# Kernel optimization log

Hardware: AMD Instinct MI355X
Metric: run time of the kernel (lower is better)

## Reference

```python
import jax, jax.numpy as jnp
import numpy as np

N, D, H = 4096, 2048, 16
DK = D // H  # 128


def setup_inputs() -> dict:
    key = jax.random.key(0)
    k0, k1, k2, k3 = jax.random.split(key, 4)
    return {
        "tokens_embedding": jax.random.normal(k0, (N, D), dtype=jnp.float32),
        "w_q": jax.random.normal(k1, (H, D, DK), dtype=jnp.float32),
        "w_k": jax.random.normal(k2, (H, D, DK), dtype=jnp.float32),
        "w_v": jax.random.normal(k3, (H, D, DK), dtype=jnp.float32),
    }


def reference(tokens_embedding, w_q, w_k, w_v):
    # Per-head projections (batched over heads): [H, N, DK]
    q = jnp.einsum('nd,hdk->hnk', tokens_embedding, w_q)
    k = jnp.einsum('nd,hdk->hnk', tokens_embedding, w_k)
    v = jnp.einsum('nd,hdk->hnk', tokens_embedding, w_v)
    # Scaled dot-product attention, softmax over keys (orig dim=1 of [N,N])
    scale = 1.0 / jnp.sqrt(jnp.float32(DK))
    scores = jnp.einsum('hnk,hmk->hnm', q, k) * scale  # [H, N, N]
    attn = jax.nn.softmax(scores, axis=-1)
    out = jnp.einsum('hnm,hmk->hnk', attn, v)  # [H, N, DK]
    # Concat heads along feature dim (head order preserved): [N, H*DK]
    return jnp.transpose(out, (1, 0, 2)).reshape(N, H * DK)
```

## Files before the change

kernel.cpp:

```cpp
#include <hip/hip_runtime.h>
#include <hip/hip_bf16.h>

#define N_TOK 4096
#define D_MODEL 2048
#define NHEAD 16
#define DKH 128

typedef __attribute__((ext_vector_type(8))) short short8v;
typedef __attribute__((ext_vector_type(4))) float f32x4;
typedef __attribute__((ext_vector_type(8))) unsigned short ush8;

static __device__ __forceinline__ unsigned short f2bf(float f) {
  unsigned int x = __float_as_uint(f);
  return (unsigned short)((x + 0x7fffu + ((x >> 16) & 1u)) >> 16);
}
static __device__ __forceinline__ float bf2f(unsigned short u) {
  return __uint_as_float(((unsigned int)u) << 16);
}

static __device__ __forceinline__ void gld16(const void* g, void* l) {
  __builtin_amdgcn_global_load_lds(
      (const __attribute__((address_space(1))) unsigned int*)g,
      (__attribute__((address_space(3))) unsigned int*)l, 16, 0, 0);
}

__global__ __launch_bounds__(256)
void split_e_kernel(const float* __restrict__ E,
                    unsigned short* __restrict__ Eh,
                    unsigned short* __restrict__ El) {
  const size_t i = ((size_t)blockIdx.x * 256 + threadIdx.x) * 8;
  const int n = (int)(i >> 11), d0 = (int)(i & 2047);
  float4 v0 = *reinterpret_cast<const float4*>(E + i);
  float4 v1 = *reinterpret_cast<const float4*>(E + i + 4);
  float f[8] = {v0.x, v0.y, v0.z, v0.w, v1.x, v1.y, v1.z, v1.w};
  ush8 hi, lo;
#pragma unroll
  for (int j = 0; j < 8; ++j) {
    unsigned short hu = f2bf(f[j]);
    hi[j] = hu;
    lo[j] = f2bf(f[j] - bf2f(hu));
  }
  const size_t off = (size_t)n * D_MODEL + (d0 ^ ((n & 7) << 3));
  *reinterpret_cast<ush8*>(Eh + off) = hi;
  *reinterpret_cast<ush8*>(El + off) = lo;
}

__global__ __launch_bounds__(256)
void split_w_kernel(const float* __restrict__ Wq, const float* __restrict__ Wk,
                    const float* __restrict__ Wv,
                    unsigned short* __restrict__ WTh,
                    unsigned short* __restrict__ WTl) {
  __shared__ float tile[64][65];
  const int t = threadIdx.x;
  const int d0 = blockIdx.x * 64;
  const int k0 = blockIdx.y * 64;
  const int mh = blockIdx.z;
  const int mat = mh >> 4, h = mh & 15;
  const float* W = (mat == 0) ? Wq : (mat == 1) ? Wk : Wv;
  const float* Wp = W + (size_t)h * D_MODEL * DKH;
  const float fac = (mat == 0) ? (1.44269504089f / sqrtf(128.0f)) : 1.0f;

  const int rr = t >> 4, c4 = (t & 15) * 4;
#pragma unroll
  for (int p = 0; p < 4; ++p) {
    float4 v = *reinterpret_cast<const float4*>(Wp + (size_t)(d0 + rr + 16 * p) * DKH + k0 + c4);
    tile[rr + 16 * p][c4 + 0] = v.x * fac;
    tile[rr + 16 * p][c4 + 1] = v.y * fac;
    tile[rr + 16 * p][c4 + 2] = v.z * fac;
    tile[rr + 16 * p][c4 + 3] = v.w * fac;
  }
  __syncthreads();
  const int dd0 = (t & 7) * 8, kl = t >> 3;
#pragma unroll
  for (int p = 0; p < 2; ++p) {
    const int kg = k0 + kl + 32 * p;
    ush8 hi, lo;
#pragma unroll
    for (int j = 0; j < 8; ++j) {
      float f = tile[dd0 + j][kl + 32 * p];
      unsigned short hu = f2bf(f);
      hi[j] = hu;
      lo[j] = f2bf(f - bf2f(hu));
    }
    const size_t base = ((size_t)(mat * NHEAD + h) * DKH + kg) * D_MODEL +
                        d0 + (dd0 ^ ((kg & 7) << 3));
    *reinterpret_cast<ush8*>(WTh + base) = hi;
    if (mat < 2) *reinterpret_cast<ush8*>(WTl + base) = lo;
  }
}

template <int MODE>
__global__ __launch_bounds__(256, 2)
void proj_gemm_kernel(const unsigned short* __restrict__ Eh,
                      const unsigned short* __restrict__ El,
                      const unsigned short* __restrict__ WTh,
                      const unsigned short* __restrict__ WTl,
                      unsigned short* __restrict__ Qhi, unsigned short* __restrict__ Qlo,
                      unsigned short* __restrict__ Khi, unsigned short* __restrict__ Klo,
                      unsigned short* __restrict__ Vt, int h0) {
  __shared__ alignas(16) unsigned short Ah[128 * 64];
  __shared__ alignas(16) unsigned short Bh[128 * 64];
  __shared__ alignas(16) unsigned short Al[MODE == 0 ? 128 * 64 : 16];
  __shared__ alignas(16) unsigned short Bl[MODE == 0 ? 128 * 64 : 16];

  const int t = threadIdx.x;
  const int nb = blockIdx.x, hl = blockIdx.y, h = h0 + hl;
  const int mat = (MODE == 0) ? blockIdx.z : 2;
  const int wv = t >> 6, lane = t & 63, fr = lane & 15, fq = lane >> 4;
  const int m0 = (wv >> 1) * 64, n0 = (wv & 1) * 64;

  const char *pAh, *pBh, *pAl = nullptr, *pBl = nullptr;
  if (MODE == 0) {
    pAh = (const char*)(Eh + (size_t)nb * 128 * D_MODEL);
    pAl = (const char*)(El + (size_t)nb * 128 * D_MODEL);
    pBh = (const char*)(WTh + ((size_t)mat * NHEAD + h) * DKH * D_MODEL);
    pBl = (const char*)(WTl + ((size_t)mat * NHEAD + h) * DKH * D_MODEL);
  } else {
    pAh = (const char*)(WTh + ((size_t)2 * NHEAD + h) * DKH * D_MODEL);
    pBh = (const char*)(Eh + (size_t)nb * 128 * D_MODEL);
  }

  f32x4 acc[4][4];
#pragma unroll
  for (int a = 0; a < 4; ++a)
#pragma unroll
    for (int b = 0; b < 4; ++b) acc[a][b] = f32x4{0.f, 0.f, 0.f, 0.f};

  for (int d0 = 0; d0 < D_MODEL; d0 += 64) {
    __syncthreads();
    {
      const size_t gb = (size_t)d0 * 2 + (size_t)(t >> 3) * 4096 + (t & 7) * 16;
#pragma unroll
      for (int j = 0; j < 4; ++j) {
        gld16(pAh + gb + (size_t)j * 32 * 4096, (char*)Ah + j * 4096 + t * 16);
        gld16(pBh + gb + (size_t)j * 32 * 4096, (char*)Bh + j * 4096 + t * 16);
      }
      if (MODE == 0) {
#pragma unroll
        for (int j = 0; j < 4; ++j) {
          gld16(pAl + gb + (size_t)j * 32 * 4096, (char*)Al + j * 4096 + t * 16);
          gld16(pBl + gb + (size_t)j * 32 * 4096, (char*)Bl + j * 4096 + t * 16);
        }
      }
    }
    __syncthreads();
    __builtin_amdgcn_s_setprio(1);
#pragma unroll
    for (int ks = 0; ks < 2; ++ks) {
      short8v ah[4], al[4];
#pragma unroll
      for (int mi = 0; mi < 4; ++mi) {
        const int r = m0 + 16 * mi + fr;
        const int off = (ks * 32 + fq * 8) ^ ((r & 7) << 3);
        ah[mi] = *reinterpret_cast<const short8v*>(&Ah[r * 64 + off]);
        if (MODE == 0) al[mi] = *reinterpret_cast<const short8v*>(&Al[r * 64 + off]);
      }
#pragma unroll
      for (int ni = 0; ni < 4; ++ni) {
        const int rn = n0 + 16 * ni + fr;
        const int offn = (ks * 32 + fq * 8) ^ ((rn & 7) << 3);
        short8v bh = *reinterpret_cast<const short8v*>(&Bh[rn * 64 + offn]);
        if (MODE == 0) {
          short8v bl = *reinterpret_cast<const short8v*>(&Bl[rn * 64 + offn]);
#pragma unroll
          for (int mi = 0; mi < 4; ++mi) {
            acc[mi][ni] = __builtin_amdgcn_mfma_f32_16x16x32_bf16(ah[mi], bh, acc[mi][ni], 0, 0, 0);
            acc[mi][ni] = __builtin_amdgcn_mfma_f32_16x16x32_bf16(ah[mi], bl, acc[mi][ni], 0, 0, 0);
            acc[mi][ni] = __builtin_amdgcn_mfma_f32_16x16x32_bf16(al[mi], bh, acc[mi][ni], 0, 0, 0);
          }
        } else {
#pragma unroll
          for (int mi = 0; mi < 4; ++mi)
            acc[mi][ni] = __builtin_amdgcn_mfma_f32_16x16x32_bf16(ah[mi], bh, acc[mi][ni], 0, 0, 0);
        }
      }
    }
    __builtin_amdgcn_s_setprio(0);
  }

  if (MODE == 0) {
    unsigned short* Ohi = (mat == 0) ? Qhi : Khi;
    unsigned short* Olo = (mat == 0) ? Qlo : Klo;
#pragma unroll
    for (int mi = 0; mi < 4; ++mi)
#pragma unroll
      for (int ni = 0; ni < 4; ++ni)
#pragma unroll
        for (int i = 0; i < 4; ++i) {
          float v = acc[mi][ni][i];
          unsigned short hu = f2bf(v);
          unsigned short lu = f2bf(v - bf2f(hu));
          int n = nb * 128 + m0 + 16 * mi + fq * 4 + i;
          int k = n0 + 16 * ni + fr;
          if (mat == 1) k ^= ((n & 7) << 3);
          size_t off = ((size_t)hl * N_TOK + n) * DKH + k;
          Ohi[off] = hu;
          Olo[off] = lu;
        }
  } else {
#pragma unroll
    for (int mi = 0; mi < 4; ++mi)
#pragma unroll
      for (int ni = 0; ni < 4; ++ni)
#pragma unroll
        for (int i = 0; i < 4; ++i) {
          int kout = m0 + 16 * mi + fq * 4 + i;
          int tn = nb * 128 + n0 + 16 * ni + fr;
          int tile = tn >> 5, key = tn & 31;
          int L = ((kout >> 1) << 6) + ((kout & 1) << 5) +
                  ((((key >> 3) ^ ((kout >> 1) & 3))) << 3) + (key & 7);
          Vt[((size_t)hl * 128 + tile) * 4096 + L] = f2bf(acc[mi][ni][i]);
        }
  }
}

__global__ __launch_bounds__(256, 2)
void attn_kernel(const unsigned short* __restrict__ Qhi,
                 const unsigned short* __restrict__ Qlo,
                 const unsigned short* __restrict__ Khi,
                 const unsigned short* __restrict__ Klo,
                 const unsigned short* __restrict__ Vt,
                 float* __restrict__ out, int h0, int HC)
{
  __shared__ alignas(16) unsigned short KhiL[2][32][128];
  __shared__ alignas(16) unsigned short KloL[2][32][128];
  __shared__ alignas(16) unsigned short VtL[2][4096];

  const int t = threadIdx.x;
  int b = blockIdx.x;
  const int nwg = 32 * HC;
  if ((nwg & 7) == 0) b = (b & 7) * (nwg >> 3) + (b >> 3);
  const int qb = b & 31;
  const int hl = b >> 5;
  const int h  = h0 + hl;
  const int wv = t >> 6, lane = t & 63;
  const int fr = lane & 15, fq = lane >> 4;
  const int q0 = qb * 128 + wv * 32;

  short8v qhi[2][4], qlo[2][4];
#pragma unroll
  for (int m = 0; m < 2; ++m) {
    const unsigned short* qp  = Qhi + ((size_t)hl * N_TOK + q0 + m * 16 + fr) * DKH + fq * 8;
    const unsigned short* qp2 = Qlo + ((size_t)hl * N_TOK + q0 + m * 16 + fr) * DKH + fq * 8;
#pragma unroll
    for (int kc = 0; kc < 4; ++kc) {
      qhi[m][kc] = *reinterpret_cast<const short8v*>(qp + kc * 32);
      qlo[m][kc] = *reinterpret_cast<const short8v*>(qp2 + kc * 32);
    }
  }

  f32x4 o[2][8];
#pragma unroll
  for (int m = 0; m < 2; ++m)
#pragma unroll
    for (int i = 0; i < 8; ++i) o[m][i] = f32x4{0.f, 0.f, 0.f, 0.f};
  float mrow[2] = {-__builtin_inff(), -__builtin_inff()};
  float lrow[2] = {0.f, 0.f};

  const char* KhiB = (const char*)(Khi + (size_t)hl * N_TOK * DKH);
  const char* KloB = (const char*)(Klo + (size_t)hl * N_TOK * DKH);
  const char* VtB  = (const char*)(Vt  + (size_t)hl * (size_t)N_TOK * DKH);
  const int toff = t * 16;
  const int ga0 = (fr + ((fq & 1) << 5)) << 2;
  const int ga1 = ga0 + 64;

  auto stage = [&](int tile, int buf) {
    const char* gk  = KhiB + (size_t)tile * 8192;
    const char* gk2 = KloB + (size_t)tile * 8192;
    const char* gv  = VtB  + (size_t)tile * 8192;
#pragma unroll
    for (int j = 0; j < 2; ++j) {
      gld16(gk  + j * 4096 + toff, (char*)&KhiL[buf][0][0] + j * 4096 + toff);
      gld16(gk2 + j * 4096 + toff, (char*)&KloL[buf][0][0] + j * 4096 + toff);
      gld16(gv  + j * 4096 + toff, (char*)&VtL[buf][0]     + j * 4096 + toff);
    }
  };

  auto compute = [&](int cur) {
    f32x4 tt[2][2];
#pragma unroll
    for (int m = 0; m < 2; ++m)
#pragma unroll
      for (int kf = 0; kf < 2; ++kf) tt[m][kf] = f32x4{0.f, 0.f, 0.f, 0.f};
    __builtin_amdgcn_s_setprio(1);
#pragma unroll
    for (int kc = 0; kc < 4; ++kc) {
      short8v khf[2], klf[2];
#pragma unroll
      for (int kf = 0; kf < 2; ++kf) {
        const int kr = kf * 16 + fr;
        const int off = (kc * 32 + fq * 8) ^ ((kr & 7) << 3);
        khf[kf] = *reinterpret_cast<const short8v*>(&KhiL[cur][kr][off]);
        klf[kf] = *reinterpret_cast<const short8v*>(&KloL[cur][kr][off]);
      }
#pragma unroll
      for (int kf = 0; kf < 2; ++kf)
#pragma unroll
        for (int m = 0; m < 2; ++m) {
          tt[m][kf] = __builtin_amdgcn_mfma_f32_16x16x32_bf16(khf[kf], qhi[m][kc], tt[m][kf], 0, 0, 0);
          tt[m][kf] = __builtin_amdgcn_mfma_f32_16x16x32_bf16(klf[kf], qhi[m][kc], tt[m][kf], 0, 0, 0);
          tt[m][kf] = __builtin_amdgcn_mfma_f32_16x16x32_bf16(khf[kf], qlo[m][kc], tt[m][kf], 0, 0, 0);
        }
    }
    __builtin_amdgcn_s_setprio(0);

    float mx[2];
#pragma unroll
    for (int m = 0; m < 2; ++m) {
      float v = fmaxf(fmaxf(fmaxf(tt[m][0][0], tt[m][0][1]), fmaxf(tt[m][0][2], tt[m][0][3])),
                      fmaxf(fmaxf(tt[m][1][0], tt[m][1][1]), fmaxf(tt[m][1][2], tt[m][1][3])));
      v = fmaxf(v, __shfl_xor(v, 16));
      v = fmaxf(v, __shfl_xor(v, 32));
      mx[m] = v;
    }
    if (__any((mx[0] > mrow[0]) | (mx[1] > mrow[1]))) {
#pragma unroll
      for (int m = 0; m < 2; ++m) {
        float mn = fmaxf(mrow[m], mx[m]);
        float al = exp2f(mrow[m] - mn);
        mrow[m] = mn;
        lrow[m] *= al;
#pragma unroll
        for (int of = 0; of < 8; ++of)
#pragma unroll
          for (int i = 0; i < 4; ++i) o[m][of][i] *= al;
      }
    }
    unsigned pp[2][2][2];
#pragma unroll
    for (int m = 0; m < 2; ++m) {
      float rs = 0.f;
#pragma unroll
      for (int kf = 0; kf < 2; ++kf)
#pragma unroll
        for (int hh = 0; hh < 2; ++hh) {
          float p0 = exp2f(tt[m][kf][2 * hh]     - mrow[m]);
          float p1 = exp2f(tt[m][kf][2 * hh + 1] - mrow[m]);
          unsigned short b0 = f2bf(p0), b1 = f2bf(p1);
          rs += bf2f(b0) + bf2f(b1);
          pp[m][kf][hh] = (unsigned)b0 | ((unsigned)b1 << 16);
        }
      rs += __shfl_xor(rs, 16);
      rs += __shfl_xor(rs, 32);
      lrow[m] += rs;
    }

    union { unsigned u[4]; short8v v; } pb[2];
#pragma unroll
    for (int m = 0; m < 2; ++m) {
      unsigned c00 = __builtin_amdgcn_ds_bpermute(ga0, pp[m][0][0]);
      unsigned c10 = __builtin_amdgcn_ds_bpermute(ga0, pp[m][1][0]);
      unsigned c01 = __builtin_amdgcn_ds_bpermute(ga0, pp[m][0][1]);
      unsigned c11 = __builtin_amdgcn_ds_bpermute(ga0, pp[m][1][1]);
      unsigned d00 = __builtin_amdgcn_ds_bpermute(ga1, pp[m][0][0]);
      unsigned d10 = __builtin_amdgcn_ds_bpermute(ga1, pp[m][1][0]);
      unsigned d01 = __builtin_amdgcn_ds_bpermute(ga1, pp[m][0][1]);
      unsigned d11 = __builtin_amdgcn_ds_bpermute(ga1, pp[m][1][1]);
      const bool hi = (fq & 2);
      pb[m].u[0] = hi ? c10 : c00;
      pb[m].u[1] = hi ? c11 : c01;
      pb[m].u[2] = hi ? d10 : d00;
      pb[m].u[3] = hi ? d11 : d01;
    }

    __builtin_amdgcn_s_setprio(1);
#pragma unroll
    for (int of = 0; of < 8; ++of) {
      const int dr = of * 16 + fr;
      const char* vp = (const char*)&VtL[cur][0] +
                       (dr >> 1) * 128 + (dr & 1) * 64 + ((fq ^ ((dr >> 1) & 3)) << 4);
      short8v av = *reinterpret_cast<const short8v*>(vp);
#pragma unroll
      for (int m = 0; m < 2; ++m)
        o[m][of] = __builtin_amdgcn_mfma_f32_16x16x32_bf16(av, pb[m].v, o[m][of], 0, 0, 0);
    }
    __builtin_amdgcn_s_setprio(0);
  };

  stage(0, 0);
  asm volatile("s_waitcnt vmcnt(0)" ::: "memory");
  __builtin_amdgcn_s_barrier();
  for (int tile = 0; tile < 127; ++tile) {
    stage(tile + 1, (tile + 1) & 1);
    asm volatile("s_waitcnt vmcnt(6)" ::: "memory");
    __builtin_amdgcn_s_barrier();
    __builtin_amdgcn_sched_barrier(0);
    compute(tile & 1);
    __builtin_amdgcn_sched_barrier(0);
    __builtin_amdgcn_s_barrier();
  }
  asm volatile("s_waitcnt vmcnt(0)" ::: "memory");
  __builtin_amdgcn_s_barrier();
  compute(1);

#pragma unroll
  for (int m = 0; m < 2; ++m) {
    float inv = 1.0f / lrow[m];
    int n = q0 + m * 16 + fr;
    float* op = out + (size_t)n * (NHEAD * DKH) + h * DKH + fq * 4;
#pragma unroll
    for (int of = 0; of < 8; ++of) {
      float4 r = make_float4(o[m][of][0] * inv, o[m][of][1] * inv,
                             o[m][of][2] * inv, o[m][of][3] * inv);
      *reinterpret_cast<float4*>(op + of * 16) = r;
    }
  }
}

extern "C" void kernel_launch(void* const* d_in, const int* in_sizes, int n_in,
                              void* d_out, int out_size, void* d_ws, size_t ws_size,
                              hipStream_t stream) {
  (void)in_sizes; (void)n_in; (void)out_size;
  const float* E  = (const float*)d_in[0];
  const float* Wq = (const float*)d_in[1];
  const float* Wk = (const float*)d_in[2];
  const float* Wv = (const float*)d_in[3];
  float* out = (float*)d_out;

  const size_t ND   = (size_t)N_TOK * D_MODEL;
  const size_t WThE = (size_t)3 * NHEAD * DKH * D_MODEL;
  const size_t WTlE = (size_t)2 * NHEAD * DKH * D_MODEL;
  const size_t phe  = (size_t)N_TOK * DKH;
  const size_t baseE = 2 * ND + WThE + WTlE;

  unsigned short* Eh  = (unsigned short*)d_ws;
  unsigned short* El  = Eh + ND;
  unsigned short* WTh = El + ND;
  unsigned short* WTl = WTh + WThE;
  unsigned short* chunk = WTl + WTlE;

  int HC = NHEAD;
  while (HC > 1 && (baseE + (size_t)HC * 5 * phe) * 2 > ws_size) HC >>= 1;

  split_e_kernel<<<dim3((unsigned)(ND / 8 / 256)), 256, 0, stream>>>(E, Eh, El);
  split_w_kernel<<<dim3(32, 2, 48), 256, 0, stream>>>(Wq, Wk, Wv, WTh, WTl);

  for (int h0 = 0; h0 < NHEAD; h0 += HC) {
    unsigned short* Qhi = chunk;
    unsigned short* Qlo = Qhi + (size_t)HC * phe;
    unsigned short* Khi = Qlo + (size_t)HC * phe;
    unsigned short* Klo = Khi + (size_t)HC * phe;
    unsigned short* Vt  = Klo + (size_t)HC * phe;
    proj_gemm_kernel<1><<<dim3(32, HC, 1), 256, 0, stream>>>(Eh, El, WTh, WTl,
                                                             Qhi, Qlo, Khi, Klo, Vt, h0);
    proj_gemm_kernel<0><<<dim3(32, HC, 2), 256, 0, stream>>>(Eh, El, WTh, WTl,
                                                             Qhi, Qlo, Khi, Klo, Vt, h0);
    attn_kernel<<<dim3(32 * HC), 256, 0, stream>>>(Qhi, Qlo, Khi, Klo, Vt, out, h0, HC);
  }
}
```

Baseline: 538.9 us.

## Split attention query rows across 8 waves with 16 rows each

```diff
diff --git a/kernel.cpp b/kernel.cpp
--- a/kernel.cpp
+++ b/kernel.cpp
@@ -214,7 +214,7 @@
   }
 }
 
-__global__ __launch_bounds__(256, 2)
+__global__ __launch_bounds__(512, 2)
 void attn_kernel(const unsigned short* __restrict__ Qhi,
                  const unsigned short* __restrict__ Qlo,
                  const unsigned short* __restrict__ Khi,
@@ -235,27 +235,24 @@
   const int h  = h0 + hl;
   const int wv = t >> 6, lane = t & 63;
   const int fr = lane & 15, fq = lane >> 4;
-  const int q0 = qb * 128 + wv * 32;
-
-  short8v qhi[2][4], qlo[2][4];
-#pragma unroll
-  for (int m = 0; m < 2; ++m) {
-    const unsigned short* qp  = Qhi + ((size_t)hl * N_TOK + q0 + m * 16 + fr) * DKH + fq * 8;
-    const unsigned short* qp2 = Qlo + ((size_t)hl * N_TOK + q0 + m * 16 + fr) * DKH + fq * 8;
+  const int q0 = qb * 128 + wv * 16;
+
+  short8v qhi[4], qlo[4];
+  {
+    const unsigned short* qp  = Qhi + ((size_t)hl * N_TOK + q0 + fr) * DKH + fq * 8;
+    const unsigned short* qp2 = Qlo + ((size_t)hl * N_TOK + q0 + fr) * DKH + fq * 8;
 #pragma unroll
     for (int kc = 0; kc < 4; ++kc) {
-      qhi[m][kc] = *reinterpret_cast<const short8v*>(qp + kc * 32);
-      qlo[m][kc] = *reinterpret_cast<const short8v*>(qp2 + kc * 32);
-    }
-  }
-
-  f32x4 o[2][8];
-#pragma unroll
-  for (int m = 0; m < 2; ++m)
-#pragma unroll
-    for (int i = 0; i < 8; ++i) o[m][i] = f32x4{0.f, 0.f, 0.f, 0.f};
-  float mrow[2] = {-__builtin_inff(), -__builtin_inff()};
-  float lrow[2] = {0.f, 0.f};
+      qhi[kc] = *reinterpret_cast<const short8v*>(qp + kc * 32);
+      qlo[kc] = *reinterpret_cast<const short8v*>(qp2 + kc * 32);
+    }
+  }
+
+  f32x4 o[8];
+#pragma unroll
+  for (int i = 0; i < 8; ++i) o[i] = f32x4{0.f, 0.f, 0.f, 0.f};
+  float mrow = -__builtin_inff();
+  float lrow = 0.f;
 
   const char* KhiB = (const char*)(Khi + (size_t)hl * N_TOK * DKH);
   const char* KloB = (const char*)(Klo + (size_t)hl * N_TOK * DKH);
@@ -265,23 +262,15 @@
   const int ga1 = ga0 + 64;
 
   auto stage = [&](int tile, int buf) {
-    const char* gk  = KhiB + (size_t)tile * 8192;
-    const char* gk2 = KloB + (size_t)tile * 8192;
-    const char* gv  = VtB  + (size_t)tile * 8192;
-#pragma unroll
-    for (int j = 0; j < 2; ++j) {
-      gld16(gk  + j * 4096 + toff, (char*)&KhiL[buf][0][0] + j * 4096 + toff);
-      gld16(gk2 + j * 4096 + toff, (char*)&KloL[buf][0][0] + j * 4096 + toff);
-      gld16(gv  + j * 4096 + toff, (char*)&VtL[buf][0]     + j * 4096 + toff);
-    }
+    gld16(KhiB + (size_t)tile * 8192 + toff, (char*)&KhiL[buf][0][0] + toff);
+    gld16(KloB + (size_t)tile * 8192 + toff, (char*)&KloL[buf][0][0] + toff);
+    gld16(VtB  + (size_t)tile * 8192 + toff, (char*)&VtL[buf][0]     + toff);
   };
 
   auto compute = [&](int cur) {
-    f32x4 tt[2][2];
-#pragma unroll
-    for (int m = 0; m < 2; ++m)
-#pragma unroll
-      for (int kf = 0; kf < 2; ++kf) tt[m][kf] = f32x4{0.f, 0.f, 0.f, 0.f};
+    f32x4 tt[2];
+#pragma unroll
+    for (int kf = 0; kf < 2; ++kf) tt[kf] = f32x4{0.f, 0.f, 0.f, 0.f};
     __builtin_amdgcn_s_setprio(1);
 #pragma unroll
     for (int kc = 0; kc < 4; ++kc) {
@@ -294,73 +283,65 @@
         klf[kf] = *reinterpret_cast<const short8v*>(&KloL[cur][kr][off]);
       }
 #pragma unroll
-      for (int kf = 0; kf < 2; ++kf)
-#pragma unroll
-        for (int m = 0; m < 2; ++m) {
-          tt[m][kf] = __builtin_amdgcn_mfma_f32_16x16x32_bf16(khf[kf], qhi[m][kc], tt[m][kf], 0, 0, 0);
-          tt[m][kf] = __builtin_amdgcn_mfma_f32_16x16x32_bf16(klf[kf], qhi[m][kc], tt[m][kf], 0, 0, 0);
-          tt[m][kf] = __builtin_amdgcn_mfma_f32_16x16x32_bf16(khf[kf], qlo[m][kc], tt[m][kf], 0, 0, 0);
-        }
+      for (int kf = 0; kf < 2; ++kf) {
+        tt[kf] = __builtin_amdgcn_mfma_f32_16x16x32_bf16(khf[kf], qhi[kc], tt[kf], 0, 0, 0);
+        tt[kf] = __builtin_amdgcn_mfma_f32_16x16x32_bf16(klf[kf], qhi[kc], tt[kf], 0, 0, 0);
+        tt[kf] = __builtin_amdgcn_mfma_f32_16x16x32_bf16(khf[kf], qlo[kc], tt[kf], 0, 0, 0);
+      }
     }
     __builtin_amdgcn_s_setprio(0);
 
-    float mx[2];
-#pragma unroll
-    for (int m = 0; m < 2; ++m) {
-      float v = fmaxf(fmaxf(fmaxf(tt[m][0][0], tt[m][0][1]), fmaxf(tt[m][0][2], tt[m][0][3])),
-                      fmaxf(fmaxf(tt[m][1][0], tt[m][1][1]), fmaxf(tt[m][1][2], tt[m][1][3])));
+    float mx;
+    {
+      float v = fmaxf(fmaxf(fmaxf(tt[0][0], tt[0][1]), fmaxf(tt[0][2], tt[0][3])),
+                      fmaxf(fmaxf(tt[1][0], tt[1][1]), fmaxf(tt[1][2], tt[1][3])));
       v = fmaxf(v, __shfl_xor(v, 16));
       v = fmaxf(v, __shfl_xor(v, 32));
-      mx[m] = v;
-    }
-    if (__any((mx[0] > mrow[0]) | (mx[1] > mrow[1]))) {
-#pragma unroll
-      for (int m = 0; m < 2; ++m) {
-        float mn = fmaxf(mrow[m], mx[m]);
-        float al = exp2f(mrow[m] - mn);
-        mrow[m] = mn;
-        lrow[m] *= al;
-#pragma unroll
-        for (int of = 0; of < 8; ++of)
-#pragma unroll
-          for (int i = 0; i < 4; ++i) o[m][of][i] *= al;
-      }
-    }
-    unsigned pp[2][2][2];
-#pragma unroll
-    for (int m = 0; m < 2; ++m) {
+      mx = v;
+    }
+    if (__any(mx > mrow)) {
+      float mn = fmaxf(mrow, mx);
+      float al = exp2f(mrow - mn);
+      mrow = mn;
+      lrow *= al;
+#pragma unroll
+      for (int of = 0; of < 8; ++of)
+#pragma unroll
+        for (int i = 0; i < 4; ++i) o[of][i] *= al;
+    }
+    unsigned pp[2][2];
+    {
       float rs = 0.f;
 #pragma unroll
       for (int kf = 0; kf < 2; ++kf)
 #pragma unroll
         for (int hh = 0; hh < 2; ++hh) {
-          float p0 = exp2f(tt[m][kf][2 * hh]     - mrow[m]);
-          float p1 = exp2f(tt[m][kf][2 * hh + 1] - mrow[m]);
+          float p0 = exp2f(tt[kf][2 * hh]     - mrow);
+          float p1 = exp2f(tt[kf][2 * hh + 1] - mrow);
           unsigned short b0 = f2bf(p0), b1 = f2bf(p1);
           rs += bf2f(b0) + bf2f(b1);
-          pp[m][kf][hh] = (unsigned)b0 | ((unsigned)b1 << 16);
+          pp[kf][hh] = (unsigned)b0 | ((unsigned)b1 << 16);
         }
       rs += __shfl_xor(rs, 16);
       rs += __shfl_xor(rs, 32);
-      lrow[m] += rs;
-    }
-
-    union { unsigned u[4]; short8v v; } pb[2];
-#pragma unroll
-    for (int m = 0; m < 2; ++m) {
-      unsigned c00 = __builtin_amdgcn_ds_bpermute(ga0, pp[m][0][0]);
-      unsigned c10 = __builtin_amdgcn_ds_bpermute(ga0, pp[m][1][0]);
-      unsigned c01 = __builtin_amdgcn_ds_bpermute(ga0, pp[m][0][1]);
-      unsigned c11 = __builtin_amdgcn_ds_bpermute(ga0, pp[m][1][1]);
-      unsigned d00 = __builtin_amdgcn_ds_bpermute(ga1, pp[m][0][0]);
-      unsigned d10 = __builtin_amdgcn_ds_bpermute(ga1, pp[m][1][0]);
-      unsigned d01 = __builtin_amdgcn_ds_bpermute(ga1, pp[m][0][1]);
-      unsigned d11 = __builtin_amdgcn_ds_bpermute(ga1, pp[m][1][1]);
+      lrow += rs;
+    }
+
+    union { unsigned u[4]; short8v v; } pb;
+    {
+      unsigned c00 = __builtin_amdgcn_ds_bpermute(ga0, pp[0][0]);
+      unsigned c10 = __builtin_amdgcn_ds_bpermute(ga0, pp[1][0]);
+      unsigned c01 = __builtin_amdgcn_ds_bpermute(ga0, pp[0][1]);
+      unsigned c11 = __builtin_amdgcn_ds_bpermute(ga0, pp[1][1]);
+      unsigned d00 = __builtin_amdgcn_ds_bpermute(ga1, pp[0][0]);
+      unsigned d10 = __builtin_amdgcn_ds_bpermute(ga1, pp[1][0]);
+      unsigned d01 = __builtin_amdgcn_ds_bpermute(ga1, pp[0][1]);
+      unsigned d11 = __builtin_amdgcn_ds_bpermute(ga1, pp[1][1]);
       const bool hi = (fq & 2);
-      pb[m].u[0] = hi ? c10 : c00;
-      pb[m].u[1] = hi ? c11 : c01;
-      pb[m].u[2] = hi ? d10 : d00;
-      pb[m].u[3] = hi ? d11 : d01;
+      pb.u[0] = hi ? c10 : c00;
+      pb.u[1] = hi ? c11 : c01;
+      pb.u[2] = hi ? d10 : d00;
+      pb.u[3] = hi ? d11 : d01;
     }
 
     __builtin_amdgcn_s_setprio(1);
@@ -370,9 +351,7 @@
       const char* vp = (const char*)&VtL[cur][0] +
                        (dr >> 1) * 128 + (dr & 1) * 64 + ((fq ^ ((dr >> 1) & 3)) << 4);
       short8v av = *reinterpret_cast<const short8v*>(vp);
-#pragma unroll
-      for (int m = 0; m < 2; ++m)
-        o[m][of] = __builtin_amdgcn_mfma_f32_16x16x32_bf16(av, pb[m].v, o[m][of], 0, 0, 0);
+      o[of] = __builtin_amdgcn_mfma_f32_16x16x32_bf16(av, pb.v, o[of], 0, 0, 0);
     }
     __builtin_amdgcn_s_setprio(0);
   };
@@ -382,7 +361,7 @@
   __builtin_amdgcn_s_barrier();
   for (int tile = 0; tile < 127; ++tile) {
     stage(tile + 1, (tile + 1) & 1);
-    asm volatile("s_waitcnt vmcnt(6)" ::: "memory");
+    asm volatile("s_waitcnt vmcnt(3)" ::: "memory");
     __builtin_amdgcn_s_barrier();
     __builtin_amdgcn_sched_barrier(0);
     compute(tile & 1);
@@ -393,15 +372,14 @@
   __builtin_amdgcn_s_barrier();
   compute(1);
 
-#pragma unroll
-  for (int m = 0; m < 2; ++m) {
-    float inv = 1.0f / lrow[m];
-    int n = q0 + m * 16 + fr;
+  {
+    float inv = 1.0f / lrow;
+    int n = q0 + fr;
     float* op = out + (size_t)n * (NHEAD * DKH) + h * DKH + fq * 4;
 #pragma unroll
     for (int of = 0; of < 8; ++of) {
-      float4 r = make_float4(o[m][of][0] * inv, o[m][of][1] * inv,
-                             o[m][of][2] * inv, o[m][of][3] * inv);
+      float4 r = make_float4(o[of][0] * inv, o[of][1] * inv,
+                             o[of][2] * inv, o[of][3] * inv);
       *reinterpret_cast<float4*>(op + of * 16) = r;
     }
   }
@@ -445,6 +423,6 @@
                                                              Qhi, Qlo, Khi, Klo, Vt, h0);
     proj_gemm_kernel<0><<<dim3(32, HC, 2), 256, 0, stream>>>(Eh, El, WTh, WTl,
                                                              Qhi, Qlo, Khi, Klo, Vt, h0);
-    attn_kernel<<<dim3(32 * HC), 256, 0, stream>>>(Qhi, Qlo, Khi, Klo, Vt, out, h0, HC);
-  }
-}
+    attn_kernel<<<dim3(32 * HC), 512, 0, stream>>>(Qhi, Qlo, Khi, Klo, Vt, out, h0, HC);
+  }
+}
```

After: 521.8 us. 3.2% less time.

## Split attention key range across two wave groups with shared-memory softmax merge

Applied to the files above, without the earlier changes.

```diff
diff --git a/kernel.cpp b/kernel.cpp
--- a/kernel.cpp
+++ b/kernel.cpp
@@ -214,7 +214,7 @@
   }
 }
 
-__global__ __launch_bounds__(256, 2)
+__global__ __launch_bounds__(512, 4)
 void attn_kernel(const unsigned short* __restrict__ Qhi,
                  const unsigned short* __restrict__ Qlo,
                  const unsigned short* __restrict__ Khi,
@@ -222,9 +222,17 @@
                  const unsigned short* __restrict__ Vt,
                  float* __restrict__ out, int h0, int HC)
 {
-  __shared__ alignas(16) unsigned short KhiL[2][32][128];
-  __shared__ alignas(16) unsigned short KloL[2][32][128];
-  __shared__ alignas(16) unsigned short VtL[2][4096];
+  __shared__ union alignas(16) {
+    struct {
+      unsigned short KhiL[64][128];
+      unsigned short KloL[64][128];
+      unsigned short VtL[8192];
+    } s;
+    struct {
+      float ob[2][32][132];
+      float mb[2][32], lb[2][32];
+    } mg;
+  } sh;
 
   const int t = threadIdx.x;
   int b = blockIdx.x;
@@ -234,8 +242,9 @@
   const int hl = b >> 5;
   const int h  = h0 + hl;
   const int wv = t >> 6, lane = t & 63;
+  const int qg = wv & 3, kh = wv >> 2;
   const int fr = lane & 15, fq = lane >> 4;
-  const int q0 = qb * 128 + wv * 32;
+  const int q0 = qb * 128 + qg * 32;
 
   short8v qhi[2][4], qlo[2][4];
 #pragma unroll
@@ -264,19 +273,21 @@
   const int ga0 = (fr + ((fq & 1) << 5)) << 2;
   const int ga1 = ga0 + 64;
 
-  auto stage = [&](int tile, int buf) {
-    const char* gk  = KhiB + (size_t)tile * 8192;
-    const char* gk2 = KloB + (size_t)tile * 8192;
-    const char* gv  = VtB  + (size_t)tile * 8192;
-#pragma unroll
-    for (int j = 0; j < 2; ++j) {
-      gld16(gk  + j * 4096 + toff, (char*)&KhiL[buf][0][0] + j * 4096 + toff);
-      gld16(gk2 + j * 4096 + toff, (char*)&KloL[buf][0][0] + j * 4096 + toff);
-      gld16(gv  + j * 4096 + toff, (char*)&VtL[buf][0]     + j * 4096 + toff);
-    }
-  };
-
-  auto compute = [&](int cur) {
+  for (int kt = 0; kt < N_TOK / 64; ++kt) {
+    __syncthreads();
+    {
+      const char* gk  = KhiB + (size_t)kt * 16384;
+      const char* gk2 = KloB + (size_t)kt * 16384;
+      const char* gv  = VtB  + (size_t)kt * 16384;
+#pragma unroll
+      for (int j = 0; j < 2; ++j) {
+        gld16(gk  + j * 8192 + toff, (char*)&sh.s.KhiL[0][0] + j * 8192 + toff);
+        gld16(gk2 + j * 8192 + toff, (char*)&sh.s.KloL[0][0] + j * 8192 + toff);
+        gld16(gv  + j * 8192 + toff, (char*)&sh.s.VtL[0]     + j * 8192 + toff);
+      }
+    }
+    __syncthreads();
+
     f32x4 tt[2][2];
 #pragma unroll
     for (int m = 0; m < 2; ++m)
@@ -288,10 +299,10 @@
       short8v khf[2], klf[2];
 #pragma unroll
       for (int kf = 0; kf < 2; ++kf) {
-        const int kr = kf * 16 + fr;
-        const int off = (kc * 32 + fq * 8) ^ ((kr & 7) << 3);
-        khf[kf] = *reinterpret_cast<const short8v*>(&KhiL[cur][kr][off]);
-        klf[kf] = *reinterpret_cast<const short8v*>(&KloL[cur][kr][off]);
+        const int kr = kh * 32 + kf * 16 + fr;
+        const int off = (kc * 32 + fq * 8) ^ ((fr & 7) << 3);
+        khf[kf] = *reinterpret_cast<const short8v*>(&sh.s.KhiL[kr][off]);
+        klf[kf] = *reinterpret_cast<const short8v*>(&sh.s.KloL[kr][off]);
       }
 #pragma unroll
       for (int kf = 0; kf < 2; ++kf)
@@ -367,7 +378,7 @@
 #pragma unroll
     for (int of = 0; of < 8; ++of) {
       const int dr = of * 16 + fr;
-      const char* vp = (const char*)&VtL[cur][0] +
+      const char* vp = (const char*)&sh.s.VtL[0] + kh * 8192 +
                        (dr >> 1) * 128 + (dr & 1) * 64 + ((fq ^ ((dr >> 1) & 3)) << 4);
       short8v av = *reinterpret_cast<const short8v*>(vp);
 #pragma unroll
@@ -375,34 +386,48 @@
         o[m][of] = __builtin_amdgcn_mfma_f32_16x16x32_bf16(av, pb[m].v, o[m][of], 0, 0, 0);
     }
     __builtin_amdgcn_s_setprio(0);
-  };
-
-  stage(0, 0);
-  asm volatile("s_waitcnt vmcnt(0)" ::: "memory");
-  __builtin_amdgcn_s_barrier();
-  for (int tile = 0; tile < 127; ++tile) {
-    stage(tile + 1, (tile + 1) & 1);
-    asm volatile("s_waitcnt vmcnt(6)" ::: "memory");
-    __builtin_amdgcn_s_barrier();
-    __builtin_amdgcn_sched_barrier(0);
-    compute(tile & 1);
-    __builtin_amdgcn_sched_barrier(0);
-    __builtin_amdgcn_s_barrier();
-  }
-  asm volatile("s_waitcnt vmcnt(0)" ::: "memory");
-  __builtin_amdgcn_s_barrier();
-  compute(1);
-
-#pragma unroll
-  for (int m = 0; m < 2; ++m) {
-    float inv = 1.0f / lrow[m];
-    int n = q0 + m * 16 + fr;
-    float* op = out + (size_t)n * (NHEAD * DKH) + h * DKH + fq * 4;
-#pragma unroll
-    for (int of = 0; of < 8; ++of) {
-      float4 r = make_float4(o[m][of][0] * inv, o[m][of][1] * inv,
-                             o[m][of][2] * inv, o[m][of][3] * inv);
-      *reinterpret_cast<float4*>(op + of * 16) = r;
+  }
+
+  for (int r = 0; r < 2; ++r) {
+    __syncthreads();
+    if (kh == 1 && (qg >> 1) == r) {
+      const int s = qg & 1;
+      if (fq == 0) {
+#pragma unroll
+        for (int m = 0; m < 2; ++m) {
+          sh.mg.mb[s][m * 16 + fr] = mrow[m];
+          sh.mg.lb[s][m * 16 + fr] = lrow[m];
+        }
+      }
+#pragma unroll
+      for (int m = 0; m < 2; ++m)
+#pragma unroll
+        for (int of = 0; of < 8; ++of)
+          *reinterpret_cast<f32x4*>(&sh.mg.ob[s][m * 16 + fr][of * 16 + fq * 4]) = o[m][of];
+    }
+    __syncthreads();
+    if (kh == 0 && (qg >> 1) == r) {
+      const int s = qg & 1;
+#pragma unroll
+      for (int m = 0; m < 2; ++m) {
+        const float mB = sh.mg.mb[s][m * 16 + fr];
+        const float lB = sh.mg.lb[s][m * 16 + fr];
+        const float ms = fmaxf(mrow[m], mB);
+        const float a  = exp2f(mrow[m] - ms);
+        const float bb = exp2f(mB - ms);
+        const float inv = 1.0f / (lrow[m] * a + lB * bb);
+        const int n = q0 + m * 16 + fr;
+        float* op = out + (size_t)n * (NHEAD * DKH) + h * DKH + fq * 4;
+#pragma unroll
+        for (int of = 0; of < 8; ++of) {
+          f32x4 oB = *reinterpret_cast<const f32x4*>(&sh.mg.ob[s][m * 16 + fr][of * 16 + fq * 4]);
+          float4 rr = make_float4((o[m][of][0] * a + oB[0] * bb) * inv,
+                                  (o[m][of][1] * a + oB[1] * bb) * inv,
+                                  (o[m][of][2] * a + oB[2] * bb) * inv,
+                                  (o[m][of][3] * a + oB[3] * bb) * inv);
+          *reinterpret_cast<float4*>(op + of * 16) = rr;
+        }
+      }
     }
   }
 }
@@ -445,6 +470,6 @@
                                                              Qhi, Qlo, Khi, Klo, Vt, h0);
     proj_gemm_kernel<0><<<dim3(32, HC, 2), 256, 0, stream>>>(Eh, El, WTh, WTl,
                                                              Qhi, Qlo, Khi, Klo, Vt, h0);
-    attn_kernel<<<dim3(32 * HC), 256, 0, stream>>>(Qhi, Qlo, Khi, Klo, Vt, out, h0, HC);
-  }
-}
+    attn_kernel<<<dim3(32 * HC), 512, 0, stream>>>(Qhi, Qlo, Khi, Klo, Vt, out, h0, HC);
+  }
+}
```

Result: slower. 885.8 us (+64.4%).
